# Performance work log

Hardware: AMD Instinct MI355X
Metric: run time of the kernel (lower is better)

## Reference

```python
import jax, jax.numpy as jnp
import numpy as np
import math


def setup_inputs() -> dict:
    key = jax.random.key(0)
    k_fm, k_x, k_y, k_w, k_h = jax.random.split(key, 5)
    C, H, W = 512, 256, 256
    N = 4096
    patch_num = 4
    pe = 2  # sqrt(patch_num)
    feature_map = jax.random.normal(k_fm, (C, H, W), dtype=jnp.float32)
    # Boxes fully inside the map with per-patch extent >= 2 so every sub-box is valid.
    min_wh = 2.0 * pe + 1.0
    x0 = jax.random.uniform(k_x, (N,), minval=0.0, maxval=W / 2 - 1.0)
    y0 = jax.random.uniform(k_y, (N,), minval=0.0, maxval=H / 2 - 1.0)
    w = jax.random.uniform(k_w, (N,), minval=min_wh, maxval=W / 2 - 2.0)
    h = jax.random.uniform(k_h, (N,), minval=min_wh, maxval=H / 2 - 2.0)
    roi_batch = jnp.stack([x0, y0, x0 + w, y0 + h], axis=1).astype(jnp.float32)
    return {"feature_map": feature_map, "roi_batch": roi_batch, "patch_num": patch_num}


def _box_indices(roi_batch, patch_num, W):
    """Rounded, clamped per-patch sub-box corners; shapes (P, N), flattened patch-major."""
    pe = int(math.isqrt(patch_num))
    xmin, ymin, xmax, ymax = (roi_batch[:, k] for k in range(4))
    i = jnp.arange(patch_num)
    ix = (i % pe).astype(roi_batch.dtype)[:, None]
    iy = (i // pe).astype(roi_batch.dtype)[:, None]
    ws = ((xmax - xmin) / pe)[None, :]
    hs = ((ymax - ymin) / pe)[None, :]
    ax = xmin[None, :] + ix * ws  # (P, N)
    ay = ymin[None, :] + iy * hs
    clampi = lambda v: jnp.clip(jnp.round(v), 0, W - 1).astype(jnp.int32)
    x0, x1 = clampi(ax), clampi(ax + ws)
    y0, y1 = clampi(ay), clampi(ay + hs)
    flat = lambda a: a.reshape(-1)  # loop order: patch outer, roi inner
    return flat(x0), flat(x1), flat(y0), flat(y1)


def reference(feature_map, roi_batch, patch_num):
    C, H, W = feature_map.shape
    x0, x1, y0, y1 = _box_indices(roi_batch, patch_num, W)
    cw = x1 - x0
    ch = y1 - y0
    mask = (cw >= 1) & (ch >= 1)  # (P*N,)
    # Integral image with zero row/col padding: S[:, y, x] = sum of fm[:, :y, :x]
    S = jnp.pad(jnp.cumsum(jnp.cumsum(feature_map, axis=1), axis=2),
                ((0, 0), (1, 0), (1, 0)))
    # Region sums via 4-corner gather: (C, B)
    sums = S[:, y1, x1] - S[:, y0, x1] - S[:, y1, x0] + S[:, y0, x0]
    area = jnp.maximum(cw * ch, 1).astype(feature_map.dtype)
    pooled = (sums / area).T  # (B, C) region means == adaptive_avg_pool2d(.,(1,1))
    pooled = pooled * mask.astype(feature_map.dtype)[:, None]
    return pooled[:, :, None, None], mask.astype(jnp.int32)
```

## Files before the change

### kernel.cpp

```cpp
#include <hip/hip_runtime.h>


#define CHN 512
#define HD  256
#define WD  256
#define SP  257
#define YCH 16
#define S1_OFF 33817088UL
#define OP_OFF 67371520UL

__global__ __launch_bounds__(256) void rowScanCF(const float* __restrict__ fm,
                                                 float* __restrict__ S1) {
    const int t = threadIdx.x, lane = t & 63, wave = t >> 6;
    const int row = blockIdx.x * 4 + wave;
    const size_t base = (size_t)row * 256 + 4 * lane;
    const float4 v = *(const float4*)(fm + base);
    const float local = ((v.x + v.y) + v.z) + v.w;
    float s = local;
    #pragma unroll
    for (int d = 1; d < 64; d <<= 1) {
        float u = __shfl_up(s, d, 64);
        if (lane >= d) s += u;
    }
    const float e = s - local;
    float4 p;
    p.x = e   + v.x;
    p.y = p.x + v.y;
    p.z = p.y + v.z;
    p.w = p.z + v.w;
    *(float4*)(S1 + base) = p;
}

__global__ __launch_bounds__(256) void colScanT(const float* __restrict__ S1,
                                                float* __restrict__ S) {
    __shared__ float T[32][132];
    const int t = threadIdx.x, lane = t & 63, wave = t >> 6;
    const int bid = blockIdx.x;
    const int xt = bid & 7, ct = (bid >> 3) & 3, k = bid >> 5;
    const int x0 = xt * 32, c0 = ct * 128;

    const int q  = lane & 7;
    const int rb = lane >> 3;
    const int cl = wave * 32 + rb * 4;
    const int xl = 4 * q;

    const int cq = t & 31;
    const int xs = t >> 5;

    const float4 z4 = make_float4(0.f, 0.f, 0.f, 0.f);
    if (k == 0) {
        #pragma unroll
        for (int m = 0; m < 4; ++m)
            *(float4*)(S + (size_t)(x0 + xs + 8 * m + 1) * CHN + c0 + 4 * cq) = z4;
        if (xt == 0 && t < 32)
            *(float4*)(S + (size_t)0 * CHN + c0 + 4 * t) = z4;
    }

    double acc[4][4];
    #pragma unroll
    for (int j = 0; j < 4; ++j)
        #pragma unroll
        for (int i = 0; i < 4; ++i) acc[j][i] = 0.0;

    const int r0 = k * YCH;
    float4 cur[4], nxt[4];
    #pragma unroll
    for (int j = 0; j < 4; ++j)
        cur[j] = *(const float4*)(S1 + ((size_t)(c0 + cl + j) << 16)
                                     + (size_t)r0 * 256 + x0 + xl);

    for (int yy = 0; yy < YCH; ++yy) {
        if (yy < YCH - 1) {
            #pragma unroll
            for (int j = 0; j < 4; ++j)
                nxt[j] = *(const float4*)(S1 + ((size_t)(c0 + cl + j) << 16)
                                             + (size_t)(r0 + yy + 1) * 256 + x0 + xl);
        }
        #pragma unroll
        for (int j = 0; j < 4; ++j) {
            acc[j][0] += (double)cur[j].x;
            acc[j][1] += (double)cur[j].y;
            acc[j][2] += (double)cur[j].z;
            acc[j][3] += (double)cur[j].w;
        }
        #pragma unroll
        for (int i = 0; i < 4; ++i) {
            float4 w;
            w.x = (float)acc[0][i];
            w.y = (float)acc[1][i];
            w.z = (float)acc[2][i];
            w.w = (float)acc[3][i];
            *(float4*)&T[xl + i][cl] = w;
        }
        __syncthreads();
        const int yS = r0 + yy + 1;
        #pragma unroll
        for (int m = 0; m < 4; ++m) {
            const int x_l = xs + 8 * m;
            const float4 o = *(const float4*)&T[x_l][4 * cq];
            *(float4*)(S + ((size_t)yS * SP + (x0 + x_l + 1)) * CHN + c0 + 4 * cq) = o;
        }
        if (xt == 0 && t < 32)
            *(float4*)(S + ((size_t)yS * SP) * CHN + c0 + 4 * t) = z4;
        __syncthreads();
        #pragma unroll
        for (int j = 0; j < 4; ++j) cur[j] = nxt[j];
    }
}

__global__ __launch_bounds__(256) void offsetK(const float* __restrict__ S,
                                               float* __restrict__ OP) {
    const int gid = blockIdx.x * 256 + threadIdx.x;
    const int c = gid & 511, x = gid >> 9;
    OP[((size_t)0 * SP + x) * CHN + c] = 0.0f;
    OP[((size_t)1 * SP + x) * CHN + c] = 0.0f;
    double run = 0.0;
    #pragma unroll
    for (int j = 0; j < 15; ++j) {
        run += (double)S[((size_t)(16 * (j + 1)) * SP + x) * CHN + c];
        OP[((size_t)(j + 2) * SP + x) * CHN + c] = (float)run;
    }
}

__global__ __launch_bounds__(256) void gatherK(const float* __restrict__ S,
                                              const float* __restrict__ OP,
                                              const float* __restrict__ roi,
                                              float* __restrict__ out,
                                              float* __restrict__ maskOut,
                                              int N) {
    const int n = blockIdx.x;
    const float xmin = roi[4 * n + 0];
    const float ymin = roi[4 * n + 1];
    const float xmax = roi[4 * n + 2];
    const float ymax = roi[4 * n + 3];

    const float wsv = __fdiv_rn(__fsub_rn(xmax, xmin), 2.0f);
    const float hsv = __fdiv_rn(__fsub_rn(ymax, ymin), 2.0f);
    const float ax1 = __fadd_rn(xmin, wsv);
    const float ay1 = __fadd_rn(ymin, hsv);
    const float lim = (float)(WD - 1);

    int rx[3], ry[3];
    rx[0] = (int)fminf(fmaxf(rintf(xmin), 0.0f), lim);
    rx[1] = (int)fminf(fmaxf(rintf(ax1), 0.0f), lim);
    rx[2] = (int)fminf(fmaxf(rintf(__fadd_rn(ax1, wsv)), 0.0f), lim);
    ry[0] = (int)fminf(fmaxf(rintf(ymin), 0.0f), lim);
    ry[1] = (int)fminf(fmaxf(rintf(ay1), 0.0f), lim);
    ry[2] = (int)fminf(fmaxf(rintf(__fadd_rn(ay1, hsv)), 0.0f), lim);

    const int t = threadIdx.x;
    float2 g[3][3];
    #pragma unroll
    for (int j = 0; j < 3; ++j) {
        const int kk = (ry[j] + 15) >> 4;
        #pragma unroll
        for (int i = 0; i < 3; ++i) {
            const float2 l = *(const float2*)(S  + ((size_t)ry[j] * SP + rx[i]) * CHN + 2 * t);
            const float2 o = *(const float2*)(OP + ((size_t)kk   * SP + rx[i]) * CHN + 2 * t);
            g[j][i] = make_float2(l.x + o.x, l.y + o.y);
        }
    }

    float m[4];
    #pragma unroll
    for (int p = 0; p < 4; ++p) {
        const int ix = p & 1, iy = p >> 1;
        const int cw = rx[ix + 1] - rx[ix];
        const int ch = ry[iy + 1] - ry[iy];
        const int maskv = (cw >= 1 && ch >= 1) ? 1 : 0;
        int areai = cw * ch; if (areai < 1) areai = 1;
        const float areaf = (float)areai;
        const float maskf = (float)maskv;
        m[p] = maskf;

        const float2 s11 = g[iy + 1][ix + 1];
        const float2 s01 = g[iy][ix + 1];
        const float2 s10 = g[iy + 1][ix];
        const float2 s00 = g[iy][ix];
        float2 o;
        o.x = __fdiv_rn(((s11.x - s01.x) - s10.x) + s00.x, areaf) * maskf;
        o.y = __fdiv_rn(((s11.y - s01.y) - s10.y) + s00.y, areaf) * maskf;
        *(float2*)(out + ((size_t)p * N + n) * CHN + 2 * t) = o;
    }
    if (t < 4) maskOut[(size_t)t * N + n] = m[t];
}

extern "C" void kernel_launch(void* const* d_in, const int* in_sizes, int n_in,
                              void* d_out, int out_size, void* d_ws, size_t ws_size,
                              hipStream_t stream) {
    const float* fm  = (const float*)d_in[0];
    const float* roi = (const float*)d_in[1];

    const int N = in_sizes[1] / 4;
    const int B = 4 * N;

    float* S  = (float*)d_ws;
    float* S1 = (float*)d_ws + S1_OFF;
    float* OP = (float*)d_ws + OP_OFF;
    float* out     = (float*)d_out;
    float* maskOut = out + (size_t)B * CHN;

    rowScanCF<<<(CHN * HD) / 4, 256, 0, stream>>>(fm, S1);
    colScanT<<<8 * 4 * 16, 256, 0, stream>>>(S1, S);
    offsetK<<<(SP * CHN) / 256, 256, 0, stream>>>(S, OP);
    gatherK<<<N, 256, 0, stream>>>(S, OP, roi, out, maskOut, N);
}
```

Measured before the change: 301.2 us.

## Fuse row and column scans into one kernel with double-buffered LDS tile

Merges the row-prefix-scan and column-scan kernels into one kernel that row-scans feature map rows in registers via wave shuffles, stages them in a double-buffered LDS tile, and accumulates column sums in float. This removes the intermediate S1 buffer's full write and re-read, and drops the second barrier per row. The y-chunk shrinks from 16 to 8 rows, giving 32 chunks, so the offset kernel and gather indexing change to match. The column accumulation switches from double to float, which can change rounding within a chunk.

```diff
diff --git a/kernel.cpp b/kernel.cpp
--- a/kernel.cpp
+++ b/kernel.cpp
@@ -5,106 +5,84 @@
 #define HD  256
 #define WD  256
 #define SP  257
-#define YCH 16
-#define S1_OFF 33817088UL
-#define OP_OFF 67371520UL
+#define YC  8
+#define NK  32
+#define OP_OFF 33817088UL
 
-__global__ __launch_bounds__(256) void rowScanCF(const float* __restrict__ fm,
-                                                 float* __restrict__ S1) {
-    const int t = threadIdx.x, lane = t & 63, wave = t >> 6;
-    const int row = blockIdx.x * 4 + wave;
-    const size_t base = (size_t)row * 256 + 4 * lane;
-    const float4 v = *(const float4*)(fm + base);
-    const float local = ((v.x + v.y) + v.z) + v.w;
-    float s = local;
-    #pragma unroll
-    for (int d = 1; d < 64; d <<= 1) {
-        float u = __shfl_up(s, d, 64);
-        if (lane >= d) s += u;
-    }
-    const float e = s - local;
-    float4 p;
-    p.x = e   + v.x;
-    p.y = p.x + v.y;
-    p.z = p.y + v.z;
-    p.w = p.z + v.w;
-    *(float4*)(S1 + base) = p;
-}
+__global__ __launch_bounds__(256) void fusedScanK(const float* __restrict__ fm,
+                                                  float* __restrict__ S) {
+    __shared__ float tile[2][32][260];
+    const int t = threadIdx.x, lane = t & 63, w = t >> 6;
+    const int c0 = blockIdx.x * 32;
+    const int k  = blockIdx.y;
+    const int y0 = k * YC;
 
-__global__ __launch_bounds__(256) void colScanT(const float* __restrict__ S1,
-                                                float* __restrict__ S) {
-    __shared__ float T[32][132];
-    const int t = threadIdx.x, lane = t & 63, wave = t >> 6;
-    const int bid = blockIdx.x;
-    const int xt = bid & 7, ct = (bid >> 3) & 3, k = bid >> 5;
-    const int x0 = xt * 32, c0 = ct * 128;
+    const int cg = t & 7;
+    const int x8 = t >> 3;
+    const float4 z4 = make_float4(0.f, 0.f, 0.f, 0.f);
 
-    const int q  = lane & 7;
-    const int rb = lane >> 3;
-    const int cl = wave * 32 + rb * 4;
-    const int xl = 4 * q;
-
-    const int cq = t & 31;
-    const int xs = t >> 5;
-
-    const float4 z4 = make_float4(0.f, 0.f, 0.f, 0.f);
     if (k == 0) {
         #pragma unroll
-        for (int m = 0; m < 4; ++m)
-            *(float4*)(S + (size_t)(x0 + xs + 8 * m + 1) * CHN + c0 + 4 * cq) = z4;
-        if (xt == 0 && t < 32)
-            *(float4*)(S + (size_t)0 * CHN + c0 + 4 * t) = z4;
+        for (int it = 0; it < 8; ++it) {
+            const int lin = it * 256 + t;
+            const int cgg = lin & 7, x = lin >> 3;
+            *(float4*)(S + (size_t)x * CHN + c0 + 4 * cgg) = z4;
+        }
     }
 
-    double acc[4][4];
+    float4 cur[8], nxt[8];
     #pragma unroll
-    for (int j = 0; j < 4; ++j)
-        #pragma unroll
-        for (int i = 0; i < 4; ++i) acc[j][i] = 0.0;
+    for (int j = 0; j < 8; ++j)
+        cur[j] = *(const float4*)(fm + ((size_t)(c0 + w * 8 + j) << 16)
+                                     + (size_t)y0 * 256 + 4 * lane);
 
-    const int r0 = k * YCH;
-    float4 cur[4], nxt[4];
+    float4 acc[8];
     #pragma unroll
-    for (int j = 0; j < 4; ++j)
-        cur[j] = *(const float4*)(S1 + ((size_t)(c0 + cl + j) << 16)
-                                     + (size_t)r0 * 256 + x0 + xl);
+    for (int m = 0; m < 8; ++m) acc[m] = z4;
 
-    for (int yy = 0; yy < YCH; ++yy) {
-        if (yy < YCH - 1) {
+    for (int y = 0; y < YC; ++y) {
+        const int buf = y & 1;
+        if (y < YC - 1) {
             #pragma unroll
-            for (int j = 0; j < 4; ++j)
-                nxt[j] = *(const float4*)(S1 + ((size_t)(c0 + cl + j) << 16)
-                                             + (size_t)(r0 + yy + 1) * 256 + x0 + xl);
+            for (int j = 0; j < 8; ++j)
+                nxt[j] = *(const float4*)(fm + ((size_t)(c0 + w * 8 + j) << 16)
+                                             + (size_t)(y0 + y + 1) * 256 + 4 * lane);
         }
         #pragma unroll
-        for (int j = 0; j < 4; ++j) {
-            acc[j][0] += (double)cur[j].x;
-            acc[j][1] += (double)cur[j].y;
-            acc[j][2] += (double)cur[j].z;
-            acc[j][3] += (double)cur[j].w;
-        }
-        #pragma unroll
-        for (int i = 0; i < 4; ++i) {
-            float4 w;
-            w.x = (float)acc[0][i];
-            w.y = (float)acc[1][i];
-            w.z = (float)acc[2][i];
-            w.w = (float)acc[3][i];
-            *(float4*)&T[xl + i][cl] = w;
+        for (int j = 0; j < 8; ++j) {
+            const float4 v = cur[j];
+            const float local = ((v.x + v.y) + v.z) + v.w;
+            float s = local;
+            #pragma unroll
+            for (int d = 1; d < 64; d <<= 1) {
+                float u = __shfl_up(s, d, 64);
+                if (lane >= d) s += u;
+            }
+            const float e = s - local;
+            float4 p;
+            p.x = e   + v.x;
+            p.y = p.x + v.y;
+            p.z = p.y + v.z;
+            p.w = p.z + v.w;
+            *(float4*)&tile[buf][w * 8 + j][4 * lane] = p;
         }
         __syncthreads();
-        const int yS = r0 + yy + 1;
+        const size_t rowb = ((size_t)(y0 + y + 1) * SP) * CHN;
         #pragma unroll
-        for (int m = 0; m < 4; ++m) {
-            const int x_l = xs + 8 * m;
-            const float4 o = *(const float4*)&T[x_l][4 * cq];
-            *(float4*)(S + ((size_t)yS * SP + (x0 + x_l + 1)) * CHN + c0 + 4 * cq) = o;
+        for (int m = 0; m < 8; ++m) {
+            const int x = x8 + 32 * m;
+            float4 a = acc[m];
+            a.x += tile[buf][4 * cg + 0][x];
+            a.y += tile[buf][4 * cg + 1][x];
+            a.z += tile[buf][4 * cg + 2][x];
+            a.w += tile[buf][4 * cg + 3][x];
+            acc[m] = a;
+            *(float4*)(S + rowb + (size_t)(x + 1) * CHN + c0 + 4 * cg) = a;
         }
-        if (xt == 0 && t < 32)
-            *(float4*)(S + ((size_t)yS * SP) * CHN + c0 + 4 * t) = z4;
-        __syncthreads();
+        if (t < 8)
+            *(float4*)(S + rowb + c0 + 4 * t) = z4;
         #pragma unroll
-        for (int j = 0; j < 4; ++j) cur[j] = nxt[j];
+        for (int j = 0; j < 8; ++j) cur[j] = nxt[j];
     }
 }
 
@@ -115,9 +93,8 @@
     OP[((size_t)0 * SP + x) * CHN + c] = 0.0f;
     OP[((size_t)1 * SP + x) * CHN + c] = 0.0f;
     double run = 0.0;
-    #pragma unroll
-    for (int j = 0; j < 15; ++j) {
-        run += (double)S[((size_t)(16 * (j + 1)) * SP + x) * CHN + c];
+    for (int j = 0; j < NK - 1; ++j) {
+        run += (double)S[((size_t)(YC * (j + 1)) * SP + x) * CHN + c];
         OP[((size_t)(j + 2) * SP + x) * CHN + c] = (float)run;
     }
 }
@@ -152,7 +129,7 @@
     float2 g[3][3];
     #pragma unroll
     for (int j = 0; j < 3; ++j) {
-        const int kk = (ry[j] + 15) >> 4;
+        const int kk = (ry[j] + YC - 1) >> 3;
         #pragma unroll
         for (int i = 0; i < 3; ++i) {
             const float2 l = *(const float2*)(S  + ((size_t)ry[j] * SP + rx[i]) * CHN + 2 * t);
@@ -195,13 +172,14 @@
     const int B = 4 * N;
 
     float* S  = (float*)d_ws;
-    float* S1 = (float*)d_ws + S1_OFF;
     float* OP = (float*)d_ws + OP_OFF;
     float* out     = (float*)d_out;
     float* maskOut = out + (size_t)B * CHN;
 
-    rowScanCF<<<(CHN * HD) / 4, 256, 0, stream>>>(fm, S1);
-    colScanT<<<8 * 4 * 16, 256, 0, stream>>>(S1, S);
+    dim3 gF(CHN / 32, NK);
+    fusedScanK<<<gF, 256, 0, stream>>>(fm, S);
+
     offsetK<<<(SP * CHN) / 256, 256, 0, stream>>>(S, OP);
+
     gatherK<<<N, 256, 0, stream>>>(S, OP, roi, out, maskOut, N);
 }
```

After: 268.7 us. 10.8% less time.
